# Optimization experiments

Measured on AMD Instinct MI355X. Metric: run time of the kernel, lower is better.

## Reference

```python
import jax, jax.numpy as jnp
import numpy as np
from jax import lax

N, H, W, C = 4, 64, 64, 256
G, K = 8, 3
Cg = C // G
PAD, STRIDE, DIL = 1, 1, 1
OFFSET_SCALE = 1.0
P = K * K


def setup_inputs() -> dict:
    key = jax.random.key(0)
    ks = jax.random.split(key, 12)
    s = 1.0 / np.sqrt(C)
    return {
        "x": jax.random.normal(ks[0], (N, H, W, C), jnp.float32),
        "in_w": jax.random.normal(ks[1], (C, C), jnp.float32) * s,
        "in_b": jnp.zeros((C,), jnp.float32),
        "out_w": jax.random.normal(ks[2], (C, C), jnp.float32) * s,
        "out_b": jnp.zeros((C,), jnp.float32),
        "off_w": jax.random.normal(ks[3], (C, G * P * 2), jnp.float32) * 0.02,
        "off_b": jax.random.normal(ks[4], (G * P * 2,), jnp.float32) * 0.1,
        "mask_w": jax.random.normal(ks[5], (C, G * P), jnp.float32) * 0.02,
        "mask_b": jnp.zeros((G * P,), jnp.float32),
        "dw_k": jax.random.normal(ks[6], (C, 1, K, K), jnp.float32) * (1.0 / K),
        "bn_g": 1.0 + 0.1 * jax.random.normal(ks[7], (C,), jnp.float32),
        "bn_b": 0.1 * jax.random.normal(ks[8], (C,), jnp.float32),
        "bn_m": 0.1 * jax.random.normal(ks[9], (C,), jnp.float32),
        "bn_v": 1.0 + 0.1 * jax.random.uniform(ks[10], (C,), jnp.float32),
    }


def _bilinear_sample(img, grid):
    # img: [B, Cc, Hi, Wi]; grid: [B, L, P, 2], (x, y) in [-1, 1]
    # grid_sample(mode='bilinear', padding_mode='zeros', align_corners=False)
    B, Cc, Hi, Wi = img.shape
    x = ((grid[..., 0] + 1.0) * Wi - 1.0) * 0.5
    y = ((grid[..., 1] + 1.0) * Hi - 1.0) * 0.5
    x0 = jnp.floor(x)
    y0 = jnp.floor(y)
    fx = x - x0
    fy = y - y0
    x0i = x0.astype(jnp.int32)
    y0i = y0.astype(jnp.int32)
    flat = img.reshape(B, Cc, Hi * Wi)
    gather = jax.vmap(lambda f, i: f[:, i])  # [Cc,HW], [L,P] -> [Cc,L,P]

    def corner(xc, yc, w):
        valid = (xc >= 0) & (xc < Wi) & (yc >= 0) & (yc < Hi)
        idx = jnp.clip(yc, 0, Hi - 1) * Wi + jnp.clip(xc, 0, Wi - 1)
        return gather(flat, idx) * (w * valid)[:, None]

    out = corner(x0i, y0i, (1.0 - fx) * (1.0 - fy))
    out = out + corner(x0i + 1, y0i, fx * (1.0 - fy))
    out = out + corner(x0i, y0i + 1, (1.0 - fx) * fy)
    out = out + corner(x0i + 1, y0i + 1, fx * fy)
    return out  # [B, Cc, L, P]


def reference(x, in_w, in_b, out_w, out_b, off_w, off_b, mask_w, mask_b,
              dw_k, bn_g, bn_b, bn_m, bn_v):
    # input_proj
    xp = x @ in_w + in_b  # [N,H,W,C]

    # depthwise conv (Conv: conv -> BN(inference) -> SiLU) on NCHW
    x1 = jnp.transpose(x, (0, 3, 1, 2))
    x1 = lax.conv_general_dilated(x1, dw_k, (1, 1), [(PAD, PAD), (PAD, PAD)],
                                  feature_group_count=C)
    x1 = (bn_g[:, None, None] * (x1 - bn_m[:, None, None])
          * lax.rsqrt(bn_v + 1e-5)[:, None, None] + bn_b[:, None, None])
    x1 = jax.nn.silu(x1)
    x1 = jnp.transpose(x1, (0, 2, 3, 1))  # NHWC

    offset = x1 @ off_w + off_b  # [N,H,W,G*P*2]
    mask = jax.nn.softmax((x1 @ mask_w + mask_b).reshape(N, H, W, G, P), -1)

    # dcnv3 core: pad input, compute sampling locations, bilinear gather
    Hi, Wi = H + 2 * PAD, W + 2 * PAD
    xpad = jnp.pad(xp, ((0, 0), (PAD, PAD), (PAD, PAD), (0, 0)))

    base = (DIL * (K - 1)) // 2 + 0.5
    ref_y = (base + jnp.arange(H, dtype=jnp.float32) * STRIDE) / Hi
    ref_x = (base + jnp.arange(W, dtype=jnp.float32) * STRIDE) / Wi
    ref = jnp.stack(jnp.meshgrid(ref_x, ref_y, indexing="xy"), -1)  # [H,W,2]

    g1 = jnp.arange(K, dtype=jnp.float32) * DIL - (DIL * (K - 1)) // 2
    gx = jnp.repeat(g1 / Wi, K)  # kx outer (torch meshgrid 'ij' order)
    gy = jnp.tile(g1 / Hi, K)    # ky inner
    grid = jnp.stack([gx, gy], -1)  # [P,2]

    norm = jnp.array([Wi, Hi], jnp.float32)
    loc = (ref[None, :, :, None, None, :]
           + grid[None, None, None, None, :, :] * OFFSET_SCALE
           + offset.reshape(N, H, W, G, P, 2) * (OFFSET_SCALE / norm))
    sgrid = 2.0 * loc - 1.0  # [N,H,W,G,P,2]

    img = xpad.reshape(N, Hi * Wi, G, Cg).transpose(0, 2, 3, 1).reshape(N * G, Cg, Hi, Wi)
    sg = sgrid.reshape(N, H * W, G, P, 2).transpose(0, 2, 1, 3, 4).reshape(N * G, H * W, P, 2)
    samples = _bilinear_sample(img, sg)  # [N*G, Cg, L, P]
    m = mask.reshape(N, H * W, G, P).transpose(0, 2, 1, 3).reshape(N * G, 1, H * W, P)
    out = (samples * m).sum(-1)  # [N*G, Cg, L]
    out = out.reshape(N, C, H * W).transpose(0, 2, 1).reshape(N, H, W, C)
    return out @ out_w + out_b
```

## Files before the change

### kernel.cpp

```cpp
#include <hip/hip_runtime.h>
#include <math.h>

#define NB   4
#define HH   64
#define WW   64
#define CCH  256
#define GG   8
#define CGC  32
#define HI   66
#define NPIX 16384
#define OMWS 256

typedef unsigned short ushort_t;
typedef __attribute__((ext_vector_type(8))) short short8;
typedef __attribute__((ext_vector_type(4))) float floatx4;

__device__ inline ushort_t f2bf(float f) {
    union { float f; unsigned u; } v; v.f = f;
    unsigned r = v.u + 0x7FFF + ((v.u >> 16) & 1);
    return (ushort_t)(r >> 16);
}
__device__ inline float bf2f(ushort_t u) {
    union { unsigned u; float f; } v; v.u = ((unsigned)u) << 16; return v.f;
}

__device__ inline void gload_lds16(const ushort_t* g, ushort_t* l) {
    __builtin_amdgcn_global_load_lds(
        (const __attribute__((address_space(1))) void*)g,
        (__attribute__((address_space(3))) void*)l, 16, 0, 0);
}

template<int MODE>
__global__ __launch_bounds__(256)
void gemm_mfma(const ushort_t* __restrict__ A, const ushort_t* __restrict__ Bt,
               const float* __restrict__ bias, void* __restrict__ outv)
{
    __shared__ ushort_t As[2][128 * 64];
    __shared__ ushort_t Bs[2][64 * 64];
    const int tid  = threadIdx.x;
    const int lane = tid & 63, wid = tid >> 6;
    const int q = lane >> 4, r = lane & 15;
    const int bid = blockIdx.x;
    const int swz = (bid & 7) * 64 + (bid >> 3);
    const int row0 = (swz >> 2) * 128, col0 = (swz & 3) * 64;

    floatx4 acc[2][4] = {};

    auto stage = [&](int buf, int kt) {
        #pragma unroll
        for (int j = 0; j < 4; ++j) {
            int gi = j * 256 + tid;
            int arow = gi >> 3, gk = gi & 7;
            gload_lds16(A + (size_t)(row0 + arow) * 256 + kt * 64 + ((gk ^ (arow & 7)) * 8),
                        &As[buf][gi * 8]);
        }
        #pragma unroll
        for (int j = 0; j < 2; ++j) {
            int gi = j * 256 + tid;
            int brow = gi >> 3, gk = gi & 7;
            gload_lds16(Bt + (size_t)(col0 + brow) * 256 + kt * 64 + ((gk ^ (brow & 7)) * 8),
                        &Bs[buf][gi * 8]);
        }
    };

    stage(0, 0);
    __syncthreads();
    int cur = 0;
    #pragma unroll 1
    for (int kt = 0; kt < 4; ++kt) {
        if (kt < 3) stage(cur ^ 1, kt + 1);
        #pragma unroll
        for (int kk = 0; kk < 2; ++kk) {
            short8 af[2], bf[4];
            const int gsw = ((kk * 4 + q) ^ (r & 7)) * 8;
            #pragma unroll
            for (int m = 0; m < 2; ++m)
                af[m] = *(const short8*)&As[cur][(wid * 32 + m * 16 + r) * 64 + gsw];
            #pragma unroll
            for (int n = 0; n < 4; ++n)
                bf[n] = *(const short8*)&Bs[cur][(n * 16 + r) * 64 + gsw];
            #pragma unroll
            for (int m = 0; m < 2; ++m)
                #pragma unroll
                for (int n = 0; n < 4; ++n)
                    acc[m][n] = __builtin_amdgcn_mfma_f32_16x16x32_bf16(
                                    af[m], bf[n], acc[m][n], 0, 0, 0);
        }
        __syncthreads();
        cur ^= 1;
    }

    #pragma unroll
    for (int m = 0; m < 2; ++m) {
        #pragma unroll
        for (int n = 0; n < 4; ++n) {
            #pragma unroll
            for (int j = 0; j < 4; ++j) {
                int row = row0 + wid * 32 + m * 16 + q * 4 + j;
                int col = col0 + n * 16 + r;
                float v = acc[m][n][j] + bias[col];
                if (MODE == 1) {
                    int nn = row >> 12, hh = (row >> 6) & 63, www = row & 63;
                    ((ushort_t*)outv)[(size_t)((nn * HI + hh + 1) * HI + (www + 1)) * CCH + col] = f2bf(v);
                } else if (MODE == 2) {
                    ((ushort_t*)outv)[(size_t)row * 256 + col] = f2bf(v);
                } else {
                    ((float*)outv)[(size_t)row * 256 + col] = v;
                }
            }
        }
    }
}

__global__ __launch_bounds__(256)
void ring_pack(ushort_t* __restrict__ xpadb,
               const float* __restrict__ in_w, const float* __restrict__ out_w,
               const float* __restrict__ off_w, const float* __restrict__ mask_w,
               const float* __restrict__ off_b, const float* __restrict__ mask_b,
               const float* __restrict__ dw_k, const float* __restrict__ bn_g,
               const float* __restrict__ bn_b, const float* __restrict__ bn_m,
               const float* __restrict__ bn_v,
               ushort_t* __restrict__ WtIn, ushort_t* __restrict__ WtOut,
               ushort_t* __restrict__ W2t, float* __restrict__ b2,
               float* __restrict__ dwkT, float* __restrict__ bnS,
               float* __restrict__ bnB)
{
    int bid = blockIdx.x;
    if (bid < NB * 260) {
        int n = bid / 260, rp = bid % 260;
        int h, w;
        if (rp < 66)       { h = 0;              w = rp; }
        else if (rp < 132) { h = 65;             w = rp - 66; }
        else if (rp < 196) { h = 1 + (rp - 132); w = 0; }
        else               { h = 1 + (rp - 196); w = 65; }
        xpadb[(size_t)((n * HI + h) * HI + w) * CCH + threadIdx.x] = 0;
        return;
    }
    int n = bid - NB * 260, k = threadIdx.x;
    WtIn [n * 256 + k] = f2bf(in_w [k * 256 + n]);
    WtOut[n * 256 + k] = f2bf(out_w[k * 256 + n]);
    float w2 = (n < 144) ? off_w[k * 144 + n]
             : (n < 216) ? mask_w[k * 72 + (n - 144)] : 0.f;
    W2t[n * 256 + k] = f2bf(w2);
    if (k == 0) b2[n] = (n < 144) ? off_b[n] : (n < 216) ? mask_b[n - 144] : 0.f;
    if (k < 9) dwkT[k * 256 + n] = dw_k[n * 9 + k];
    if (k == 9) {
        float s = bn_g[n] * rsqrtf(bn_v[n] + 1e-5f);
        bnS[n] = s;
        bnB[n] = bn_b[n] - bn_m[n] * s;
    }
}

__global__ __launch_bounds__(256)
void dw_bn_silu(const float* __restrict__ x, const float* __restrict__ dwkT,
                const float* __restrict__ bnS, const float* __restrict__ bnB,
                ushort_t* __restrict__ x1b, ushort_t* __restrict__ xb)
{
    const int lane = threadIdx.x & 63, wid = threadIdx.x >> 6;
    const int pix = blockIdx.x * 4 + wid;
    const int n = pix >> 12, hw = pix & 4095, h = hw >> 6, w = hw & 63;
    const int c4 = lane << 2;

    const float4 cv = *reinterpret_cast<const float4*>(x + (size_t)pix * CCH + c4);
    ushort_t xo[4] = { f2bf(cv.x), f2bf(cv.y), f2bf(cv.z), f2bf(cv.w) };
    *reinterpret_cast<ushort4*>(xb + (size_t)pix * CCH + c4) = *reinterpret_cast<ushort4*>(xo);

    const float4 kc = *reinterpret_cast<const float4*>(dwkT + 4 * 256 + c4);
    float ax = cv.x * kc.x, ay = cv.y * kc.y, az = cv.z * kc.z, aw = cv.w * kc.w;

    #pragma unroll
    for (int tap = 0; tap < 9; ++tap) {
        if (tap == 4) continue;
        int hh = h + tap / 3 - 1, ww = w + tap % 3 - 1;
        if ((unsigned)hh < HH && (unsigned)ww < WW) {
            const float4 v = *reinterpret_cast<const float4*>(
                x + (size_t)((n * HH + hh) * WW + ww) * CCH + c4);
            const float4 kk = *reinterpret_cast<const float4*>(dwkT + tap * 256 + c4);
            ax += v.x * kk.x; ay += v.y * kk.y; az += v.z * kk.z; aw += v.w * kk.w;
        }
    }
    const float4 s = *reinterpret_cast<const float4*>(bnS + c4);
    const float4 b = *reinterpret_cast<const float4*>(bnB + c4);
    float yx = ax * s.x + b.x, yy = ay * s.y + b.y;
    float yz = az * s.z + b.z, yw = aw * s.w + b.w;
    yx = yx / (1.f + __expf(-yx));
    yy = yy / (1.f + __expf(-yy));
    yz = yz / (1.f + __expf(-yz));
    yw = yw / (1.f + __expf(-yw));
    ushort_t o[4] = { f2bf(yx), f2bf(yy), f2bf(yz), f2bf(yw) };
    *reinterpret_cast<ushort4*>(x1b + (size_t)pix * CCH + c4) = *reinterpret_cast<ushort4*>(o);
}

__global__ __launch_bounds__(256)
void dcn_sample(const ushort_t* __restrict__ xpadb, const ushort_t* __restrict__ om,
                ushort_t* __restrict__ coreb)
{
    const int tid = threadIdx.x;
    const int pix = blockIdx.x * 8 + (tid >> 5);
    const int l   = tid & 31;
    const int g = l >> 2, c8 = (l & 3) << 3;
    const int n = pix >> 12, hw = pix & 4095, h = hw >> 6, w = hw & 63;
    const ushort_t* __restrict__ omp = om + (size_t)pix * OMWS;

    float lg[9], mx = -1e30f;
    #pragma unroll
    for (int p = 0; p < 9; ++p) { lg[p] = bf2f(omp[144 + g * 9 + p]); mx = fmaxf(mx, lg[p]); }
    float s = 0.f;
    #pragma unroll
    for (int p = 0; p < 9; ++p) { lg[p] = __expf(lg[p] - mx); s += lg[p]; }
    const float inv = 1.f / s;

    const ushort_t* __restrict__ img = xpadb + (size_t)n * HI * HI * CCH + g * CGC + c8;
    float acc[8] = {};
    #pragma unroll
    for (int p = 0; p < 9; ++p) {
        float ox = bf2f(omp[g * 18 + p * 2 + 0]);
        float oy = bf2f(omp[g * 18 + p * 2 + 1]);
        float xi = (float)(w + (p / 3)) + ox;
        float yi = (float)(h + (p % 3)) + oy;
        float x0f = floorf(xi), y0f = floorf(yi);
        int x0 = (int)x0f, y0 = (int)y0f;
        float fx = xi - x0f, fy = yi - y0f;
        float wgt = lg[p] * inv;
        float cw[4] = { (1.f - fx) * (1.f - fy) * wgt, fx * (1.f - fy) * wgt,
                        (1.f - fx) * fy * wgt,         fx * fy * wgt };
        #pragma unroll
        for (int cr = 0; cr < 4; ++cr) {
            int xc = x0 + (cr & 1), yc = y0 + (cr >> 1);
            if ((unsigned)xc < HI && (unsigned)yc < HI) {
                short8 raw = *reinterpret_cast<const short8*>(img + (size_t)(yc * HI + xc) * CCH);
                float wc = cw[cr];
                #pragma unroll
                for (int j = 0; j < 8; ++j) acc[j] += wc * bf2f((ushort_t)raw[j]);
            }
        }
    }
    ushort_t o[8];
    #pragma unroll
    for (int j = 0; j < 8; ++j) o[j] = f2bf(acc[j]);
    *reinterpret_cast<short8*>(coreb + (size_t)pix * CCH + g * CGC + c8) =
        *reinterpret_cast<short8*>(o);
}

extern "C" void kernel_launch(void* const* d_in, const int* in_sizes, int n_in,
                              void* d_out, int out_size, void* d_ws, size_t ws_size,
                              hipStream_t stream) {
    const float* x      = (const float*)d_in[0];
    const float* in_w   = (const float*)d_in[1];
    const float* in_b   = (const float*)d_in[2];
    const float* out_w  = (const float*)d_in[3];
    const float* out_b  = (const float*)d_in[4];
    const float* off_w  = (const float*)d_in[5];
    const float* off_b  = (const float*)d_in[6];
    const float* mask_w = (const float*)d_in[7];
    const float* mask_b = (const float*)d_in[8];
    const float* dw_k   = (const float*)d_in[9];
    const float* bn_g   = (const float*)d_in[10];
    const float* bn_b   = (const float*)d_in[11];
    const float* bn_m   = (const float*)d_in[12];
    const float* bn_v   = (const float*)d_in[13];

    ushort_t* xpadb = (ushort_t*)d_ws;
    ushort_t* xb    = xpadb + 4460544;
    ushort_t* x1b   = xb + 4194304;
    ushort_t* coreb = x1b + 4194304;
    ushort_t* offm  = coreb + 4194304;
    ushort_t* WtIn  = offm + 4194304;
    ushort_t* WtOut = WtIn + 65536;
    ushort_t* W2t   = WtOut + 65536;
    float*    b2    = (float*)(W2t + 65536);
    float*    dwkT  = b2 + 256;
    float*    bnS   = dwkT + 9 * 256;
    float*    bnB   = bnS + 256;

    ring_pack<<<NB * 260 + 256, 256, 0, stream>>>(xpadb,
        in_w, out_w, off_w, mask_w, off_b, mask_b,
        dw_k, bn_g, bn_b, bn_m, bn_v,
        WtIn, WtOut, W2t, b2, dwkT, bnS, bnB);

    dw_bn_silu<<<NPIX / 4, 256, 0, stream>>>(x, dwkT, bnS, bnB, x1b, xb);

    gemm_mfma<1><<<512, 256, 0, stream>>>(xb, WtIn, in_b, xpadb);

    gemm_mfma<2><<<512, 256, 0, stream>>>(x1b, W2t, b2, offm);

    dcn_sample<<<NPIX / 8, 256, 0, stream>>>(xpadb, offm, coreb);

    gemm_mfma<0><<<512, 256, 0, stream>>>(coreb, WtOut, out_b, (float*)d_out);
}
```

Baseline: 66.60 us.

## Fuse prep with depthwise conv and merge the two input GEMMs into one launch

Combines the zero-ring/weight-pack kernel with the depthwise conv + BN + SiLU kernel, computing BN scale and reading dw weights directly instead of through precomputed tables. Merges the in-projection and offset/mask GEMMs into a single 1024-block launch sharing a templated GEMM body. The aim is to cut kernel launch overhead and inter-kernel gaps, and to give the GPU more concurrent blocks. In exchange, dw weight loads become strided per-thread scalar reads and rsqrt is recomputed per pixel.

```diff
diff --git a/kernel.cpp b/kernel.cpp
--- a/kernel.cpp
+++ b/kernel.cpp
@@ -31,18 +31,14 @@
 }
 
 template<int MODE>
-__global__ __launch_bounds__(256)
-void gemm_mfma(const ushort_t* __restrict__ A, const ushort_t* __restrict__ Bt,
-               const float* __restrict__ bias, void* __restrict__ outv)
-{
-    __shared__ ushort_t As[2][128 * 64];
-    __shared__ ushort_t Bs[2][64 * 64];
+__device__ __forceinline__
+void gemm_body(const ushort_t* __restrict__ A, const ushort_t* __restrict__ Bt,
+               const float* __restrict__ bias, void* __restrict__ outv,
+               ushort_t* As, ushort_t* Bs, int row0, int col0)
+{
     const int tid  = threadIdx.x;
     const int lane = tid & 63, wid = tid >> 6;
     const int q = lane >> 4, r = lane & 15;
-    const int bid = blockIdx.x;
-    const int swz = (bid & 7) * 64 + (bid >> 3);
-    const int row0 = (swz >> 2) * 128, col0 = (swz & 3) * 64;
 
     floatx4 acc[2][4] = {};
 
@@ -52,14 +48,14 @@
             int gi = j * 256 + tid;
             int arow = gi >> 3, gk = gi & 7;
             gload_lds16(A + (size_t)(row0 + arow) * 256 + kt * 64 + ((gk ^ (arow & 7)) * 8),
-                        &As[buf][gi * 8]);
+                        &As[buf * 128 * 64 + gi * 8]);
         }
         #pragma unroll
         for (int j = 0; j < 2; ++j) {
             int gi = j * 256 + tid;
             int brow = gi >> 3, gk = gi & 7;
             gload_lds16(Bt + (size_t)(col0 + brow) * 256 + kt * 64 + ((gk ^ (brow & 7)) * 8),
-                        &Bs[buf][gi * 8]);
+                        &Bs[buf * 64 * 64 + gi * 8]);
         }
     };
 
@@ -75,10 +71,10 @@
             const int gsw = ((kk * 4 + q) ^ (r & 7)) * 8;
             #pragma unroll
             for (int m = 0; m < 2; ++m)
-                af[m] = *(const short8*)&As[cur][(wid * 32 + m * 16 + r) * 64 + gsw];
+                af[m] = *(const short8*)&As[cur * 128 * 64 + (wid * 32 + m * 16 + r) * 64 + gsw];
             #pragma unroll
             for (int n = 0; n < 4; ++n)
-                bf[n] = *(const short8*)&Bs[cur][(n * 16 + r) * 64 + gsw];
+                bf[n] = *(const short8*)&Bs[cur * 64 * 64 + (n * 16 + r) * 64 + gsw];
             #pragma unroll
             for (int m = 0; m < 2; ++m)
                 #pragma unroll
@@ -112,20 +108,58 @@
     }
 }
 
+__device__ __forceinline__ void swz512(int tbid, int& row0, int& col0) {
+    int swz = (tbid & 7) * 64 + (tbid >> 3);
+    row0 = (swz >> 2) * 128;
+    col0 = (swz & 3) * 64;
+}
+
 __global__ __launch_bounds__(256)
-void ring_pack(ushort_t* __restrict__ xpadb,
-               const float* __restrict__ in_w, const float* __restrict__ out_w,
-               const float* __restrict__ off_w, const float* __restrict__ mask_w,
-               const float* __restrict__ off_b, const float* __restrict__ mask_b,
-               const float* __restrict__ dw_k, const float* __restrict__ bn_g,
-               const float* __restrict__ bn_b, const float* __restrict__ bn_m,
-               const float* __restrict__ bn_v,
-               ushort_t* __restrict__ WtIn, ushort_t* __restrict__ WtOut,
-               ushort_t* __restrict__ W2t, float* __restrict__ b2,
-               float* __restrict__ dwkT, float* __restrict__ bnS,
-               float* __restrict__ bnB)
-{
+void gemm_in_off(const ushort_t* __restrict__ xb, const ushort_t* __restrict__ WtIn,
+                 const float* __restrict__ in_b, ushort_t* __restrict__ xpadb,
+                 const ushort_t* __restrict__ x1b, const ushort_t* __restrict__ W2t,
+                 const float* __restrict__ b2, ushort_t* __restrict__ offm)
+{
+    __shared__ ushort_t As[2 * 128 * 64];
+    __shared__ ushort_t Bs[2 * 64 * 64];
     int bid = blockIdx.x;
+    int row0, col0;
+    if (bid < 512) {
+        swz512(bid, row0, col0);
+        gemm_body<1>(xb, WtIn, in_b, xpadb, As, Bs, row0, col0);
+    } else {
+        swz512(bid - 512, row0, col0);
+        gemm_body<2>(x1b, W2t, b2, offm, As, Bs, row0, col0);
+    }
+}
+
+__global__ __launch_bounds__(256)
+void gemm_out(const ushort_t* __restrict__ A, const ushort_t* __restrict__ Bt,
+              const float* __restrict__ bias, float* __restrict__ out)
+{
+    __shared__ ushort_t As[2 * 128 * 64];
+    __shared__ ushort_t Bs[2 * 64 * 64];
+    int row0, col0;
+    swz512(blockIdx.x, row0, col0);
+    gemm_body<0>(A, Bt, bias, out, As, Bs, row0, col0);
+}
+
+__global__ __launch_bounds__(256)
+void prep_dw(const float* __restrict__ x,
+             const float* __restrict__ in_w, const float* __restrict__ out_w,
+             const float* __restrict__ off_w, const float* __restrict__ mask_w,
+             const float* __restrict__ off_b, const float* __restrict__ mask_b,
+             const float* __restrict__ dw_k, const float* __restrict__ bn_g,
+             const float* __restrict__ bn_b, const float* __restrict__ bn_m,
+             const float* __restrict__ bn_v,
+             ushort_t* __restrict__ xpadb,
+             ushort_t* __restrict__ WtIn, ushort_t* __restrict__ WtOut,
+             ushort_t* __restrict__ W2t, float* __restrict__ b2,
+             ushort_t* __restrict__ x1b, ushort_t* __restrict__ xb)
+{
+    const int bid = blockIdx.x;
+    const int tid = threadIdx.x;
+
     if (bid < NB * 260) {
         int n = bid / 260, rp = bid % 260;
         int h, w;
@@ -133,31 +167,22 @@
         else if (rp < 132) { h = 65;             w = rp - 66; }
         else if (rp < 196) { h = 1 + (rp - 132); w = 0; }
         else               { h = 1 + (rp - 196); w = 65; }
-        xpadb[(size_t)((n * HI + h) * HI + w) * CCH + threadIdx.x] = 0;
+        xpadb[(size_t)((n * HI + h) * HI + w) * CCH + tid] = 0;
         return;
     }
-    int n = bid - NB * 260, k = threadIdx.x;
-    WtIn [n * 256 + k] = f2bf(in_w [k * 256 + n]);
-    WtOut[n * 256 + k] = f2bf(out_w[k * 256 + n]);
-    float w2 = (n < 144) ? off_w[k * 144 + n]
-             : (n < 216) ? mask_w[k * 72 + (n - 144)] : 0.f;
-    W2t[n * 256 + k] = f2bf(w2);
-    if (k == 0) b2[n] = (n < 144) ? off_b[n] : (n < 216) ? mask_b[n - 144] : 0.f;
-    if (k < 9) dwkT[k * 256 + n] = dw_k[n * 9 + k];
-    if (k == 9) {
-        float s = bn_g[n] * rsqrtf(bn_v[n] + 1e-5f);
-        bnS[n] = s;
-        bnB[n] = bn_b[n] - bn_m[n] * s;
-    }
-}
-
-__global__ __launch_bounds__(256)
-void dw_bn_silu(const float* __restrict__ x, const float* __restrict__ dwkT,
-                const float* __restrict__ bnS, const float* __restrict__ bnB,
-                ushort_t* __restrict__ x1b, ushort_t* __restrict__ xb)
-{
-    const int lane = threadIdx.x & 63, wid = threadIdx.x >> 6;
-    const int pix = blockIdx.x * 4 + wid;
+    if (bid < NB * 260 + 256) {
+        int n = bid - NB * 260, k = tid;
+        WtIn [n * 256 + k] = f2bf(in_w [k * 256 + n]);
+        WtOut[n * 256 + k] = f2bf(out_w[k * 256 + n]);
+        float w2 = (n < 144) ? off_w[k * 144 + n]
+                 : (n < 216) ? mask_w[k * 72 + (n - 144)] : 0.f;
+        W2t[n * 256 + k] = f2bf(w2);
+        if (k == 0) b2[n] = (n < 144) ? off_b[n] : (n < 216) ? mask_b[n - 144] : 0.f;
+        return;
+    }
+
+    const int lane = tid & 63, wvid = tid >> 6;
+    const int pix = (bid - (NB * 260 + 256)) * 4 + wvid;
     const int n = pix >> 12, hw = pix & 4095, h = hw >> 6, w = hw & 63;
     const int c4 = lane << 2;
 
@@ -165,24 +190,30 @@
     ushort_t xo[4] = { f2bf(cv.x), f2bf(cv.y), f2bf(cv.z), f2bf(cv.w) };
     *reinterpret_cast<ushort4*>(xb + (size_t)pix * CCH + c4) = *reinterpret_cast<ushort4*>(xo);
 
-    const float4 kc = *reinterpret_cast<const float4*>(dwkT + 4 * 256 + c4);
-    float ax = cv.x * kc.x, ay = cv.y * kc.y, az = cv.z * kc.z, aw = cv.w * kc.w;
-
+    float ax = 0.f, ay = 0.f, az = 0.f, aw = 0.f;
     #pragma unroll
     for (int tap = 0; tap < 9; ++tap) {
-        if (tap == 4) continue;
         int hh = h + tap / 3 - 1, ww = w + tap % 3 - 1;
-        if ((unsigned)hh < HH && (unsigned)ww < WW) {
+        float k0 = dw_k[(c4 + 0) * 9 + tap];
+        float k1 = dw_k[(c4 + 1) * 9 + tap];
+        float k2 = dw_k[(c4 + 2) * 9 + tap];
+        float k3 = dw_k[(c4 + 3) * 9 + tap];
+        if (tap == 4) {
+            ax += cv.x * k0; ay += cv.y * k1; az += cv.z * k2; aw += cv.w * k3;
+        } else if ((unsigned)hh < HH && (unsigned)ww < WW) {
             const float4 v = *reinterpret_cast<const float4*>(
                 x + (size_t)((n * HH + hh) * WW + ww) * CCH + c4);
-            const float4 kk = *reinterpret_cast<const float4*>(dwkT + tap * 256 + c4);
-            ax += v.x * kk.x; ay += v.y * kk.y; az += v.z * kk.z; aw += v.w * kk.w;
-        }
-    }
-    const float4 s = *reinterpret_cast<const float4*>(bnS + c4);
-    const float4 b = *reinterpret_cast<const float4*>(bnB + c4);
-    float yx = ax * s.x + b.x, yy = ay * s.y + b.y;
-    float yz = az * s.z + b.z, yw = aw * s.w + b.w;
+            ax += v.x * k0; ay += v.y * k1; az += v.z * k2; aw += v.w * k3;
+        }
+    }
+    const float4 g4 = *reinterpret_cast<const float4*>(bn_g + c4);
+    const float4 v4 = *reinterpret_cast<const float4*>(bn_v + c4);
+    const float4 m4 = *reinterpret_cast<const float4*>(bn_m + c4);
+    const float4 bb4 = *reinterpret_cast<const float4*>(bn_b + c4);
+    float sx = g4.x * rsqrtf(v4.x + 1e-5f), sy = g4.y * rsqrtf(v4.y + 1e-5f);
+    float sz = g4.z * rsqrtf(v4.z + 1e-5f), sw = g4.w * rsqrtf(v4.w + 1e-5f);
+    float yx = (ax - m4.x) * sx + bb4.x, yy = (ay - m4.y) * sy + bb4.y;
+    float yz = (az - m4.z) * sz + bb4.z, yw = (aw - m4.w) * sw + bb4.w;
     yx = yx / (1.f + __expf(-yx));
     yy = yy / (1.f + __expf(-yy));
     yz = yz / (1.f + __expf(-yz));
@@ -269,22 +300,15 @@
     ushort_t* WtOut = WtIn + 65536;
     ushort_t* W2t   = WtOut + 65536;
     float*    b2    = (float*)(W2t + 65536);
-    float*    dwkT  = b2 + 256;
-    float*    bnS   = dwkT + 9 * 256;
-    float*    bnB   = bnS + 256;
-
-    ring_pack<<<NB * 260 + 256, 256, 0, stream>>>(xpadb,
+
+    prep_dw<<<NB * 260 + 256 + NPIX / 4, 256, 0, stream>>>(x,
         in_w, out_w, off_w, mask_w, off_b, mask_b,
         dw_k, bn_g, bn_b, bn_m, bn_v,
-        WtIn, WtOut, W2t, b2, dwkT, bnS, bnB);
-
-    dw_bn_silu<<<NPIX / 4, 256, 0, stream>>>(x, dwkT, bnS, bnB, x1b, xb);
-
-    gemm_mfma<1><<<512, 256, 0, stream>>>(xb, WtIn, in_b, xpadb);
-
-    gemm_mfma<2><<<512, 256, 0, stream>>>(x1b, W2t, b2, offm);
+        xpadb, WtIn, WtOut, W2t, b2, x1b, xb);
+
+    gemm_in_off<<<1024, 256, 0, stream>>>(xb, WtIn, in_b, xpadb, x1b, W2t, b2, offm);
 
     dcn_sample<<<NPIX / 8, 256, 0, stream>>>(xpadb, offm, coreb);
 
-    gemm_mfma<0><<<512, 256, 0, stream>>>(coreb, WtOut, out_b, (float*)d_out);
-}
+    gemm_out<<<512, 256, 0, stream>>>(coreb, WtOut, out_b, (float*)d_out);
+}
```

Result: slower. 91.19 us (+36.9%).
